# Performance work log

Hardware: AMD Instinct MI355X
Metric: run time of the kernel (lower is better)

## Reference

```python
import jax, jax.numpy as jnp
import numpy as np

N_NODES = 50000


def gat_layer(x, src, dst, W, att_s, att_d, b, concat):
    # PyG GATConv (eval mode): h = x W reshaped to [N, H, C]
    H, C = att_s.shape
    h = (x @ W).reshape(-1, H, C)                      # [N, H, C]
    a_s = (h * att_s).sum(-1)                          # [N, H]
    a_d = (h * att_d).sum(-1)                          # [N, H]
    e = jax.nn.leaky_relu(a_s[src] + a_d[dst], 0.2)    # [E, H]
    # scatter-softmax over destination nodes
    m = jax.ops.segment_max(e, dst, num_segments=N_NODES)
    alpha = jnp.exp(e - m[dst])
    denom = jax.ops.segment_sum(alpha, dst, num_segments=N_NODES)
    alpha = alpha / denom[dst]                         # [E, H]
    msg = h[src] * alpha[:, :, None]                   # [E, H, C]
    out = jax.ops.segment_sum(msg, dst, num_segments=N_NODES)  # [N, H, C]
    out = out.reshape(N_NODES, H * C) if concat else out.mean(axis=1)
    return out + b


def setup_inputs() -> dict:
    key = jax.random.key(0)
    ks = jax.random.split(key, 16)
    F_IN, HID, HEADS, NCLS, E = 512, 64, 4, 40, 800000
    x = jax.random.normal(ks[0], (N_NODES, F_IN), dtype=jnp.float32)
    edge_index = jax.random.randint(ks[1], (2, E), 0, N_NODES, dtype=jnp.int32)

    def glorot(k, shape):
        fan = shape[0]
        return jax.random.normal(k, shape, dtype=jnp.float32) / np.sqrt(fan)

    d1 = HID * HEADS  # 256
    return {
        "x": x,
        "edge_index": edge_index,
        "W1": glorot(ks[2], (F_IN, d1)),
        "as1": glorot(ks[3], (HEADS, HID)),
        "ad1": glorot(ks[4], (HEADS, HID)),
        "b1": jnp.zeros((d1,), jnp.float32),
        "W2": glorot(ks[5], (d1, d1)),
        "as2": glorot(ks[6], (HEADS, HID)),
        "ad2": glorot(ks[7], (HEADS, HID)),
        "b2": jnp.zeros((d1,), jnp.float32),
        "W3": glorot(ks[8], (d1, NCLS)),
        "as3": glorot(ks[9], (1, NCLS)),
        "ad3": glorot(ks[10], (1, NCLS)),
        "b3": jnp.zeros((NCLS,), jnp.float32),
    }


def reference(x, edge_index, W1, as1, ad1, b1, W2, as2, ad2, b2, W3, as3, ad3, b3):
    # add self-loops (PyG GATConv default)
    loops = jnp.arange(N_NODES, dtype=edge_index.dtype)
    src = jnp.concatenate([edge_index[0], loops])
    dst = jnp.concatenate([edge_index[1], loops])
    h = jax.nn.elu(gat_layer(x, src, dst, W1, as1, ad1, b1, True))
    h = jax.nn.elu(gat_layer(h, src, dst, W2, as2, ad2, b2, True))
    out = gat_layer(h, src, dst, W3, as3, ad3, b3, False)
    return out
```

## Files before the change

kernel.cpp:

```cpp
#include <hip/hip_runtime.h>
#include <stdint.h>

#define NN 50000
#define NB 196

typedef unsigned short u16;
typedef _Float16 f16;
typedef __attribute__((ext_vector_type(8))) _Float16 half8;
typedef __attribute__((ext_vector_type(4))) _Float16 half4;
typedef __attribute__((ext_vector_type(4))) float f32x4;

__device__ __forceinline__ void gload_lds16(const void* gsrc, void* ldst){
  __builtin_amdgcn_global_load_lds(
      (const __attribute__((address_space(1))) unsigned int*)gsrc,
      (__attribute__((address_space(3))) unsigned int*)ldst,
      16, 0, 0);
}


__global__ void count_k(const int* __restrict__ dst, int* __restrict__ cnt, int E){
  int i = blockIdx.x * 256 + threadIdx.x;
  int tot = E + NN;
  if (i >= tot) return;
  int d = (i < E) ? dst[i] : (i - E);
  atomicAdd(&cnt[d], 1);
}

__global__ __launch_bounds__(256) void scan_part_k(const int* __restrict__ cnt,
                                                   int* __restrict__ bsum){
  __shared__ int lds[256];
  int tid = threadIdx.x;
  int idx = blockIdx.x * 256 + tid;
  lds[tid] = (idx < NN) ? cnt[idx] : 0;
  __syncthreads();
#pragma unroll
  for (int off = 128; off >= 1; off >>= 1){
    if (tid < off) lds[tid] += lds[tid + off];
    __syncthreads();
  }
  if (tid == 0) bsum[blockIdx.x] = lds[0];
}

__global__ __launch_bounds__(256) void scan_top_k(const int* __restrict__ bsum,
                                                  int* __restrict__ boff,
                                                  int* __restrict__ row_ptr){
  __shared__ int lds[256];
  int tid = threadIdx.x;
  int v = (tid < NB) ? bsum[tid] : 0;
  lds[tid] = v;
  __syncthreads();
#pragma unroll
  for (int off = 1; off < 256; off <<= 1){
    int t = (tid >= off) ? lds[tid - off] : 0;
    __syncthreads();
    lds[tid] += t;
    __syncthreads();
  }
  if (tid < NB) boff[tid] = lds[tid] - v;
  if (tid == 255) row_ptr[NN] = lds[255];
}

__global__ __launch_bounds__(256) void scan_fin_k(const int* __restrict__ cnt,
                                                  const int* __restrict__ boff,
                                                  int* __restrict__ row_ptr,
                                                  int* __restrict__ cursor){
  __shared__ int lds[256];
  int tid = threadIdx.x;
  int idx = blockIdx.x * 256 + tid;
  int v = (idx < NN) ? cnt[idx] : 0;
  lds[tid] = v;
  __syncthreads();
#pragma unroll
  for (int off = 1; off < 256; off <<= 1){
    int t = (tid >= off) ? lds[tid - off] : 0;
    __syncthreads();
    lds[tid] += t;
    __syncthreads();
  }
  if (idx < NN){
    int r = boff[blockIdx.x] + lds[tid] - v;
    row_ptr[idx] = r;
    cursor[idx]  = r;
  }
}

__global__ void scatter_k(const int* __restrict__ src, const int* __restrict__ dst,
                          int* __restrict__ cursor, int* __restrict__ csr, int E){
  int i = blockIdx.x * 256 + threadIdx.x;
  int tot = E + NN;
  if (i >= tot) return;
  int s, d;
  if (i < E){ s = src[i]; d = dst[i]; } else { s = i - E; d = i - E; }
  int pos = atomicAdd(&cursor[d], 1);
  csr[pos] = s;
}


__global__ void transpose_k(const float* __restrict__ W, f16* __restrict__ Wt, int K, int N){
  int i = blockIdx.x * 256 + threadIdx.x;
  if (i >= K * N) return;
  int n = i / K, k = i - n * K;
  Wt[i] = (f16)W[k * N + n];
}


template<bool A_FP32>
__global__ __launch_bounds__(512) void gemm_tile3_k(const void* __restrict__ Aptr,
                                                    const f16* __restrict__ Bt,
                                                    f16* __restrict__ C,
                                                    const float* __restrict__ atts,
                                                    const float* __restrict__ attd,
                                                    float* __restrict__ a_s,
                                                    float* __restrict__ a_d,
                                                    int M, int N, int K){
  constexpr int ABYTES = A_FP32 ? 8192 : 4096;
  constexpr int STEPB  = ABYTES + 8192;
  __shared__ __attribute__((aligned(16))) char lds[2 * STEPB];

  const int tid  = threadIdx.x;
  const int wave = tid >> 6, lane = tid & 63;
  const int quad = lane >> 4, l16 = lane & 15;
  const int wm = wave >> 1, wn = wave & 1;
  const int m0 = blockIdx.x * 64, n0 = blockIdx.y * 128;
  const int sc_l = lane >> 4, r_l = lane & 15;

  size_t bsrc = (size_t)(n0 + wave * 16 + r_l) * K + sc_l * 8;
  const int bdst = wave * 1024;
  size_t asrc; int adst; bool a_active = true;
  {
    int mt = wave & 3;
    int row = m0 + mt * 16 + r_l; if (row > M - 1) row = M - 1;
    if constexpr (A_FP32){
      int hp = wave >> 2;
      asrc = (size_t)row * K + sc_l * 8 + hp * 4;
      adst = hp * 4096 + mt * 1024;
    } else {
      asrc = (size_t)row * K + sc_l * 8;
      adst = mt * 1024;
      a_active = (wave < 4);
    }
  }

  auto stage = [&](int buf, int k0){
    char* Ab = lds + buf * STEPB;
    char* Bb = Ab + ABYTES;
    if constexpr (A_FP32){
      gload_lds16((const float*)Aptr + asrc + k0, Ab + adst);
    } else {
      if (a_active) gload_lds16((const f16*)Aptr + asrc + k0, Ab + adst);
    }
    gload_lds16(Bt + bsrc + k0, Bb + bdst);
  };

  f32x4 acc[4] = {};

  stage(0, 0);
  asm volatile("s_waitcnt vmcnt(0)" ::: "memory");
  __syncthreads();

  const int nk = K >> 5;
  int cur = 0;
  for (int t = 0; t < nk; ++t){
    if (t + 1 < nk) stage(cur ^ 1, (t + 1) << 5);

    char* Ab = lds + cur * STEPB;
    char* Bb = Ab + ABYTES;
    half8 af;
    if constexpr (A_FP32){
      const f32x4 lo = *(const f32x4*)(Ab + (wm * 64 + lane) * 16);
      const f32x4 hi = *(const f32x4*)(Ab + 4096 + (wm * 64 + lane) * 16);
      af[0] = (f16)lo.x; af[1] = (f16)lo.y; af[2] = (f16)lo.z; af[3] = (f16)lo.w;
      af[4] = (f16)hi.x; af[5] = (f16)hi.y; af[6] = (f16)hi.z; af[7] = (f16)hi.w;
    } else {
      af = *(const half8*)(Ab + (wm * 64 + lane) * 16);
    }
    half8 bf[4];
#pragma unroll
    for (int j = 0; j < 4; ++j)
      bf[j] = *(const half8*)(Bb + ((wn * 4 + j) * 64 + lane) * 16);
#pragma unroll
    for (int j = 0; j < 4; ++j)
      acc[j] = __builtin_amdgcn_mfma_f32_16x16x32_f16(af, bf[j], acc[j], 0, 0, 0);

    __syncthreads();
    cur ^= 1;
  }

  const int head = blockIdx.y * 2 + wn;
  float sA[4], dA[4];
#pragma unroll
  for (int j = 0; j < 4; ++j){
    sA[j] = atts[head * 64 + j * 16 + l16];
    dA[j] = attd[head * 64 + j * 16 + l16];
  }
#pragma unroll
  for (int r = 0; r < 4; ++r){
    int mm = m0 + wm * 16 + quad * 4 + r;
    float vs = 0.f, vd = 0.f;
#pragma unroll
    for (int j = 0; j < 4; ++j){
      float v = acc[j][r];
      vs += v * sA[j];
      vd += v * dA[j];
      int n = n0 + (wn * 4 + j) * 16 + l16;
      if (mm < M) C[(size_t)mm * N + n] = (f16)v;
    }
#pragma unroll
    for (int off = 8; off >= 1; off >>= 1){
      vs += __shfl_xor(vs, off);
      vd += __shfl_xor(vd, off);
    }
    if (l16 == 0 && mm < M){
      a_s[mm * 4 + head] = vs;
      a_d[mm * 4 + head] = vd;
    }
  }
}


__global__ __launch_bounds__(256) void gemm_n40_k(const f16* __restrict__ A,
                                                  const f16* __restrict__ Bt,
                                                  f16* __restrict__ C,
                                                  const float* __restrict__ atts,
                                                  const float* __restrict__ attd,
                                                  float* __restrict__ a_s,
                                                  float* __restrict__ a_d,
                                                  int M, int K){
  constexpr int ABYTES = 4096;
  constexpr int BBYTES = 3072;
  constexpr int STEPB  = ABYTES + BBYTES;
  __shared__ __attribute__((aligned(16))) char lds[2 * STEPB];

  const int tid  = threadIdx.x;
  const int wave = tid >> 6, lane = tid & 63;
  const int quad = lane >> 4, l16 = lane & 15;
  const int m0 = blockIdx.x * 64;
  const int sc_l = lane >> 4, r_l = lane & 15;

  int arow = m0 + wave * 16 + r_l; if (arow > M - 1) arow = M - 1;
  const size_t asrc = (size_t)arow * K + sc_l * 8;
  const int adst = wave * 1024;
  int brow = wave * 16 + r_l; if (brow > 39) brow = 39;
  const size_t bsrc = (size_t)brow * K + sc_l * 8;
  const int bdst = wave * 1024;
  const bool b_active = (wave < 3);

  auto stage = [&](int buf, int k0){
    char* Ab = lds + buf * STEPB;
    char* Bb = Ab + ABYTES;
    gload_lds16(A + asrc + k0, Ab + adst);
    if (b_active) gload_lds16(Bt + bsrc + k0, Bb + bdst);
  };

  f32x4 acc[3] = {};
  stage(0, 0);
  asm volatile("s_waitcnt vmcnt(0)" ::: "memory");
  __syncthreads();

  const int nk = K >> 5;
  int cur = 0;
  for (int t = 0; t < nk; ++t){
    if (t + 1 < nk) stage(cur ^ 1, (t + 1) << 5);
    char* Ab = lds + cur * STEPB;
    char* Bb = Ab + ABYTES;
    half8 af = *(const half8*)(Ab + (wave * 64 + lane) * 16);
    half8 bf[3];
#pragma unroll
    for (int j = 0; j < 3; ++j)
      bf[j] = *(const half8*)(Bb + (j * 64 + lane) * 16);
#pragma unroll
    for (int j = 0; j < 3; ++j)
      acc[j] = __builtin_amdgcn_mfma_f32_16x16x32_f16(af, bf[j], acc[j], 0, 0, 0);
    __syncthreads();
    cur ^= 1;
  }

  float sA[3], dA[3];
#pragma unroll
  for (int j = 0; j < 3; ++j){
    int n = j * 16 + l16;
    sA[j] = (n < 40) ? atts[n] : 0.f;
    dA[j] = (n < 40) ? attd[n] : 0.f;
  }
#pragma unroll
  for (int r = 0; r < 4; ++r){
    int mm = m0 + wave * 16 + quad * 4 + r;
    float vs = 0.f, vd = 0.f;
#pragma unroll
    for (int j = 0; j < 3; ++j){
      float v = acc[j][r];
      vs += v * sA[j];
      vd += v * dA[j];
      int n = j * 16 + l16;
      if (mm < M && n < 40) C[(size_t)mm * 40 + n] = (f16)v;
    }
#pragma unroll
    for (int off = 8; off >= 1; off >>= 1){
      vs += __shfl_xor(vs, off);
      vd += __shfl_xor(vd, off);
    }
    if (l16 == 0 && mm < M){
      a_s[mm] = vs;
      a_d[mm] = vd;
    }
  }
}


__device__ __forceinline__ float lrelu(float e){ return e > 0.f ? e : 0.2f * e; }

__global__ __launch_bounds__(256) void agg4_k(const f16* __restrict__ h,
                                              const float* __restrict__ a_s,
                                              const float* __restrict__ a_d,
                                              const int* __restrict__ row_ptr,
                                              const int* __restrict__ csr,
                                              const float* __restrict__ bias,
                                              f16* __restrict__ out){
  int w = blockIdx.x * 4 + (threadIdx.x >> 6);
  if (w >= NN) return;
  const int lane = threadIdx.x & 63;
  const int head = lane >> 4;
  const char* hb = (const char*)h;
  const uint32_t hoff_lane = (uint32_t)lane << 3;
  const float ad = a_d[w * 4 + head];
  const int beg = row_ptr[w], end = row_ptr[w + 1], endm1 = end - 1;

  float denom = 0.f, acc0 = 0.f, acc1 = 0.f, acc2 = 0.f, acc3 = 0.f;

  float ce[4]; half4 chv[4];
  float ne[4]; half4 nhv[4];

  auto ldgrp = [&](int base, float* EV, half4* HV){
#pragma unroll
    for (int q = 0; q < 4; ++q){
      int idx = base + q; idx = idx < endm1 ? idx : endm1;
      int s = csr[idx];
      EV[q] = a_s[(s << 2) + head];
      HV[q] = *(const half4*)(hb + (((uint32_t)s << 9) | hoff_lane));
    }
  };

  ldgrp(beg, ce, chv);
  int base = beg;
  while (true){
    bool more = base + 4 < end;
    if (more) ldgrp(base + 4, ne, nhv);
    int rem = end - base;
#pragma unroll
    for (int q = 0; q < 4; ++q){
      float al = __expf(lrelu(ce[q] + ad));
      al = (q < rem) ? al : 0.f;
      denom += al;
      acc0 += al * (float)chv[q].x;
      acc1 += al * (float)chv[q].y;
      acc2 += al * (float)chv[q].z;
      acc3 += al * (float)chv[q].w;
    }
    if (!more) break;
#pragma unroll
    for (int q = 0; q < 4; ++q){ ce[q] = ne[q]; chv[q] = nhv[q]; }
    base += 4;
  }

  float inv = 1.f / fmaxf(denom, 1e-30f);
  float o0 = acc0 * inv + bias[lane * 4 + 0];
  float o1 = acc1 * inv + bias[lane * 4 + 1];
  float o2 = acc2 * inv + bias[lane * 4 + 2];
  float o3 = acc3 * inv + bias[lane * 4 + 3];
  o0 = o0 > 0.f ? o0 : __expf(o0) - 1.f;
  o1 = o1 > 0.f ? o1 : __expf(o1) - 1.f;
  o2 = o2 > 0.f ? o2 : __expf(o2) - 1.f;
  o3 = o3 > 0.f ? o3 : __expf(o3) - 1.f;
  half4 r; r.x = (f16)o0; r.y = (f16)o1; r.z = (f16)o2; r.w = (f16)o3;
  *(half4*)(out + (size_t)w * 256 + lane * 4) = r;
}

__global__ __launch_bounds__(256) void agg1_k(const f16* __restrict__ h,
                                              const float* __restrict__ a_s,
                                              const float* __restrict__ a_d,
                                              const int* __restrict__ row_ptr,
                                              const int* __restrict__ csr,
                                              const float* __restrict__ bias,
                                              float* __restrict__ out){
  int w = blockIdx.x * 4 + (threadIdx.x >> 6);
  if (w >= NN) return;
  const int lane = threadIdx.x & 63;
  const int cl = (lane < 40) ? lane : 0;
  const float ad = a_d[w];
  const int beg = row_ptr[w], end = row_ptr[w + 1], endm1 = end - 1;

  float denom = 0.f, acc = 0.f;
  float ce[4], chv[4];
  float ne[4], nhv[4];

  auto ldgrp = [&](int base, float* EV, float* HV){
#pragma unroll
    for (int q = 0; q < 4; ++q){
      int idx = base + q; idx = idx < endm1 ? idx : endm1;
      int s = csr[idx];
      EV[q] = a_s[s];
      HV[q] = (float)h[(size_t)s * 40 + cl];
    }
  };

  ldgrp(beg, ce, chv);
  int base = beg;
  while (true){
    bool more = base + 4 < end;
    if (more) ldgrp(base + 4, ne, nhv);
    int rem = end - base;
#pragma unroll
    for (int q = 0; q < 4; ++q){
      float al = __expf(lrelu(ce[q] + ad));
      al = (q < rem) ? al : 0.f;
      denom += al;
      acc += al * chv[q];
    }
    if (!more) break;
#pragma unroll
    for (int q = 0; q < 4; ++q){ ce[q] = ne[q]; chv[q] = nhv[q]; }
    base += 4;
  }

  if (lane < 40){
    float o = acc / fmaxf(denom, 1e-30f) + bias[lane];
    out[(size_t)w * 40 + lane] = o;
  }
}


extern "C" void kernel_launch(void* const* d_in, const int* in_sizes, int n_in,
                              void* d_out, int out_size, void* d_ws, size_t ws_size,
                              hipStream_t stream){
  const float* x   = (const float*)d_in[0];
  const int*   ei  = (const int*)d_in[1];
  const float* W1  = (const float*)d_in[2];
  const float* as1 = (const float*)d_in[3];
  const float* ad1 = (const float*)d_in[4];
  const float* b1  = (const float*)d_in[5];
  const float* W2  = (const float*)d_in[6];
  const float* as2 = (const float*)d_in[7];
  const float* ad2 = (const float*)d_in[8];
  const float* b2  = (const float*)d_in[9];
  const float* W3  = (const float*)d_in[10];
  const float* as3 = (const float*)d_in[11];
  const float* ad3 = (const float*)d_in[12];
  const float* b3  = (const float*)d_in[13];

  const int E = in_sizes[1] / 2;
  const int ETOT = E + NN;
  const int* src_arr = ei;
  const int* dst_arr = ei + E;

  char* ws = (char*)d_ws;
  size_t off = 0;
  auto alloc = [&](size_t bytes) -> void* {
    void* p = ws + off; off += (bytes + 255) & ~(size_t)255; return p;
  };
  int*   cnt     = (int*)  alloc((size_t)NN * 4);
  int*   row_ptr = (int*)  alloc((size_t)(NN + 1) * 4);
  int*   cursor  = (int*)  alloc((size_t)NN * 4);
  int*   csr     = (int*)  alloc((size_t)ETOT * 4);
  int*   bsum    = (int*)  alloc((size_t)256 * 4);
  int*   boff    = (int*)  alloc((size_t)256 * 4);
  f16*   W1t     = (f16*)  alloc((size_t)512 * 256 * 2);
  f16*   W2t     = (f16*)  alloc((size_t)256 * 256 * 2);
  f16*   W3t     = (f16*)  alloc((size_t)256 * 40 * 2);
  float* a_s     = (float*)alloc((size_t)NN * 4 * 4);
  float* a_d     = (float*)alloc((size_t)NN * 4 * 4);
  f16*   hbuf    = (f16*)  alloc((size_t)NN * 256 * 2);
  f16*   xbuf    = (f16*)  alloc((size_t)NN * 256 * 2);
  (void)ws_size; (void)n_in; (void)out_size;

  hipMemsetAsync(cnt, 0, (size_t)NN * 4, stream);
  int egrid = (ETOT + 255) / 256;
  count_k    <<<egrid, 256, 0, stream>>>(dst_arr, cnt, E);
  scan_part_k<<<NB, 256, 0, stream>>>(cnt, bsum);
  scan_top_k <<<1, 256, 0, stream>>>(bsum, boff, row_ptr);
  scan_fin_k <<<NB, 256, 0, stream>>>(cnt, boff, row_ptr, cursor);
  scatter_k  <<<egrid, 256, 0, stream>>>(src_arr, dst_arr, cursor, csr, E);

  transpose_k<<<(512 * 256 + 255) / 256, 256, 0, stream>>>(W1, W1t, 512, 256);
  transpose_k<<<(256 * 256 + 255) / 256, 256, 0, stream>>>(W2, W2t, 256, 256);
  transpose_k<<<(256 * 40  + 255) / 256, 256, 0, stream>>>(W3, W3t, 256, 40);

  dim3 blk512(512);
  dim3 blk(256);
  dim3 gT((NN + 63) / 64, 2);
  dim3 gC((NN + 63) / 64, 1);
  int nodeblocks = (NN + 3) / 4;

  gemm_tile3_k<true> <<<gT, blk512, 0, stream>>>(x, W1t, hbuf, as1, ad1, a_s, a_d, NN, 256, 512);
  agg4_k <<<nodeblocks, blk, 0, stream>>>(hbuf, a_s, a_d, row_ptr, csr, b1, xbuf);

  gemm_tile3_k<false><<<gT, blk512, 0, stream>>>(xbuf, W2t, hbuf, as2, ad2, a_s, a_d, NN, 256, 256);
  agg4_k <<<nodeblocks, blk, 0, stream>>>(hbuf, a_s, a_d, row_ptr, csr, b2, xbuf);

  gemm_n40_k<<<gC, blk, 0, stream>>>(xbuf, W3t, hbuf, as3, ad3, a_s, a_d, NN, 256);
  agg1_k <<<nodeblocks, blk, 0, stream>>>(hbuf, a_s, a_d, row_ptr, csr, b3, (float*)d_out);
}
```

Before: 534.1 us.

## Replace LDS-staged GEMMs with direct register-prefetched global loads

The three GEMM kernels no longer stage A and B tiles through LDS with async global-to-LDS loads and block barriers. Each lane now loads its MFMA fragments straight from global memory into registers, with one-step register prefetch and a fully unrolled compile-time K loop. The big GEMMs also move from 512-thread 64x128 tiles to 256-thread 32x128 tiles. This removes LDS traffic and __syncthreads, but each wave now fetches its own B fragments, so reuse moves from LDS to the cache hierarchy and global load volume may rise.

Measured after the change: 643.4 us. 1.2x slower.

```diff
diff --git a/kernel.cpp b/kernel.cpp
--- a/kernel.cpp
+++ b/kernel.cpp
@@ -9,13 +9,6 @@
 typedef __attribute__((ext_vector_type(8))) _Float16 half8;
 typedef __attribute__((ext_vector_type(4))) _Float16 half4;
 typedef __attribute__((ext_vector_type(4))) float f32x4;
-
-__device__ __forceinline__ void gload_lds16(const void* gsrc, void* ldst){
-  __builtin_amdgcn_global_load_lds(
-      (const __attribute__((address_space(1))) unsigned int*)gsrc,
-      (__attribute__((address_space(3))) unsigned int*)ldst,
-      16, 0, 0);
-}
 
 
 __global__ void count_k(const int* __restrict__ dst, int* __restrict__ cnt, int E){
@@ -104,89 +97,78 @@
 }
 
 
-template<bool A_FP32>
-__global__ __launch_bounds__(512) void gemm_tile3_k(const void* __restrict__ Aptr,
-                                                    const f16* __restrict__ Bt,
-                                                    f16* __restrict__ C,
-                                                    const float* __restrict__ atts,
-                                                    const float* __restrict__ attd,
-                                                    float* __restrict__ a_s,
-                                                    float* __restrict__ a_d,
-                                                    int M, int N, int K){
-  constexpr int ABYTES = A_FP32 ? 8192 : 4096;
-  constexpr int STEPB  = ABYTES + 8192;
-  __shared__ __attribute__((aligned(16))) char lds[2 * STEPB];
-
+template<bool A_FP32, int K>
+__global__ __launch_bounds__(256) void gemm_direct_k(const void* __restrict__ Aptr,
+                                                     const f16* __restrict__ Bt,
+                                                     f16* __restrict__ C,
+                                                     const float* __restrict__ atts,
+                                                     const float* __restrict__ attd,
+                                                     float* __restrict__ a_s,
+                                                     float* __restrict__ a_d,
+                                                     int M){
+  constexpr int NK = K / 32;
+  constexpr int N  = 256;
   const int tid  = threadIdx.x;
   const int wave = tid >> 6, lane = tid & 63;
   const int quad = lane >> 4, l16 = lane & 15;
   const int wm = wave >> 1, wn = wave & 1;
-  const int m0 = blockIdx.x * 64, n0 = blockIdx.y * 128;
-  const int sc_l = lane >> 4, r_l = lane & 15;
-
-  size_t bsrc = (size_t)(n0 + wave * 16 + r_l) * K + sc_l * 8;
-  const int bdst = wave * 1024;
-  size_t asrc; int adst; bool a_active = true;
-  {
-    int mt = wave & 3;
-    int row = m0 + mt * 16 + r_l; if (row > M - 1) row = M - 1;
-    if constexpr (A_FP32){
-      int hp = wave >> 2;
-      asrc = (size_t)row * K + sc_l * 8 + hp * 4;
-      adst = hp * 4096 + mt * 1024;
-    } else {
-      asrc = (size_t)row * K + sc_l * 8;
-      adst = mt * 1024;
-      a_active = (wave < 4);
-    }
-  }
-
-  auto stage = [&](int buf, int k0){
-    char* Ab = lds + buf * STEPB;
-    char* Bb = Ab + ABYTES;
-    if constexpr (A_FP32){
-      gload_lds16((const float*)Aptr + asrc + k0, Ab + adst);
-    } else {
-      if (a_active) gload_lds16((const f16*)Aptr + asrc + k0, Ab + adst);
-    }
-    gload_lds16(Bt + bsrc + k0, Bb + bdst);
-  };
+  const int bid = blockIdx.x;
+  const int m0 = (bid >> 1) * 32;
+  const int n0 = (bid & 1) * 128;
+  const int r  = lane & 15, ck = lane >> 4;
+
+  int arow = m0 + wm * 16 + r; if (arow > M - 1) arow = M - 1;
+  const float* A32 = (const float*)Aptr;
+  const f16*   A16 = (const f16*)Aptr;
+  const size_t abase = (size_t)arow * K + ck * 8;
+  size_t bbase[4];
+#pragma unroll
+  for (int j = 0; j < 4; ++j)
+    bbase[j] = (size_t)(n0 + wn * 64 + j * 16 + r) * K + ck * 8;
 
   f32x4 acc[4] = {};
 
-  stage(0, 0);
-  asm volatile("s_waitcnt vmcnt(0)" ::: "memory");
-  __syncthreads();
-
-  const int nk = K >> 5;
-  int cur = 0;
-  for (int t = 0; t < nk; ++t){
-    if (t + 1 < nk) stage(cur ^ 1, (t + 1) << 5);
-
-    char* Ab = lds + cur * STEPB;
-    char* Bb = Ab + ABYTES;
+  f32x4 plo = {}, phi = {}; half8 pa = {};
+  half8 pb[4];
+  if constexpr (A_FP32){
+    plo = *(const f32x4*)(A32 + abase);
+    phi = *(const f32x4*)(A32 + abase + 4);
+  } else {
+    pa = *(const half8*)(A16 + abase);
+  }
+#pragma unroll
+  for (int j = 0; j < 4; ++j) pb[j] = *(const half8*)(Bt + bbase[j]);
+
+#pragma unroll
+  for (int t = 0; t < NK; ++t){
+    f32x4 nlo = {}, nhi = {}; half8 na = {}; half8 nb[4] = {};
+    if (t + 1 < NK){
+      const int ko = (t + 1) * 32;
+      if constexpr (A_FP32){
+        nlo = *(const f32x4*)(A32 + abase + ko);
+        nhi = *(const f32x4*)(A32 + abase + ko + 4);
+      } else {
+        na = *(const half8*)(A16 + abase + ko);
+      }
+#pragma unroll
+      for (int j = 0; j < 4; ++j) nb[j] = *(const half8*)(Bt + bbase[j] + ko);
+    }
     half8 af;
     if constexpr (A_FP32){
-      const f32x4 lo = *(const f32x4*)(Ab + (wm * 64 + lane) * 16);
-      const f32x4 hi = *(const f32x4*)(Ab + 4096 + (wm * 64 + lane) * 16);
-      af[0] = (f16)lo.x; af[1] = (f16)lo.y; af[2] = (f16)lo.z; af[3] = (f16)lo.w;
-      af[4] = (f16)hi.x; af[5] = (f16)hi.y; af[6] = (f16)hi.z; af[7] = (f16)hi.w;
+      af[0] = (f16)plo.x; af[1] = (f16)plo.y; af[2] = (f16)plo.z; af[3] = (f16)plo.w;
+      af[4] = (f16)phi.x; af[5] = (f16)phi.y; af[6] = (f16)phi.z; af[7] = (f16)phi.w;
     } else {
-      af = *(const half8*)(Ab + (wm * 64 + lane) * 16);
-    }
-    half8 bf[4];
+      af = pa;
+    }
 #pragma unroll
     for (int j = 0; j < 4; ++j)
-      bf[j] = *(const half8*)(Bb + ((wn * 4 + j) * 64 + lane) * 16);
-#pragma unroll
-    for (int j = 0; j < 4; ++j)
-      acc[j] = __builtin_amdgcn_mfma_f32_16x16x32_f16(af, bf[j], acc[j], 0, 0, 0);
-
-    __syncthreads();
-    cur ^= 1;
-  }
-
-  const int head = blockIdx.y * 2 + wn;
+      acc[j] = __builtin_amdgcn_mfma_f32_16x16x32_f16(af, pb[j], acc[j], 0, 0, 0);
+    plo = nlo; phi = nhi; pa = na;
+#pragma unroll
+    for (int j = 0; j < 4; ++j) pb[j] = nb[j];
+  }
+
+  const int head = (bid & 1) * 2 + wn;
   float sA[4], dA[4];
 #pragma unroll
   for (int j = 0; j < 4; ++j){
@@ -194,12 +176,12 @@
     dA[j] = attd[head * 64 + j * 16 + l16];
   }
 #pragma unroll
-  for (int r = 0; r < 4; ++r){
-    int mm = m0 + wm * 16 + quad * 4 + r;
+  for (int rr = 0; rr < 4; ++rr){
+    int mm = m0 + wm * 16 + quad * 4 + rr;
     float vs = 0.f, vd = 0.f;
 #pragma unroll
     for (int j = 0; j < 4; ++j){
-      float v = acc[j][r];
+      float v = acc[j][rr];
       vs += v * sA[j];
       vd += v * dA[j];
       int n = n0 + (wn * 4 + j) * 16 + l16;
@@ -218,61 +200,52 @@
 }
 
 
-__global__ __launch_bounds__(256) void gemm_n40_k(const f16* __restrict__ A,
-                                                  const f16* __restrict__ Bt,
-                                                  f16* __restrict__ C,
-                                                  const float* __restrict__ atts,
-                                                  const float* __restrict__ attd,
-                                                  float* __restrict__ a_s,
-                                                  float* __restrict__ a_d,
-                                                  int M, int K){
-  constexpr int ABYTES = 4096;
-  constexpr int BBYTES = 3072;
-  constexpr int STEPB  = ABYTES + BBYTES;
-  __shared__ __attribute__((aligned(16))) char lds[2 * STEPB];
-
+__global__ __launch_bounds__(256) void gemm_n40d_k(const f16* __restrict__ A,
+                                                   const f16* __restrict__ Bt,
+                                                   f16* __restrict__ C,
+                                                   const float* __restrict__ atts,
+                                                   const float* __restrict__ attd,
+                                                   float* __restrict__ a_s,
+                                                   float* __restrict__ a_d,
+                                                   int M){
+  constexpr int K = 256, NK = K / 32;
   const int tid  = threadIdx.x;
   const int wave = tid >> 6, lane = tid & 63;
   const int quad = lane >> 4, l16 = lane & 15;
   const int m0 = blockIdx.x * 64;
-  const int sc_l = lane >> 4, r_l = lane & 15;
-
-  int arow = m0 + wave * 16 + r_l; if (arow > M - 1) arow = M - 1;
-  const size_t asrc = (size_t)arow * K + sc_l * 8;
-  const int adst = wave * 1024;
-  int brow = wave * 16 + r_l; if (brow > 39) brow = 39;
-  const size_t bsrc = (size_t)brow * K + sc_l * 8;
-  const int bdst = wave * 1024;
-  const bool b_active = (wave < 3);
-
-  auto stage = [&](int buf, int k0){
-    char* Ab = lds + buf * STEPB;
-    char* Bb = Ab + ABYTES;
-    gload_lds16(A + asrc + k0, Ab + adst);
-    if (b_active) gload_lds16(Bt + bsrc + k0, Bb + bdst);
-  };
+  const int r  = lane & 15, ck = lane >> 4;
+
+  int arow = m0 + wave * 16 + r; if (arow > M - 1) arow = M - 1;
+  const size_t abase = (size_t)arow * K + ck * 8;
+  size_t bbase[3];
+#pragma unroll
+  for (int j = 0; j < 3; ++j){
+    int brow = j * 16 + r; if (brow > 39) brow = 39;
+    bbase[j] = (size_t)brow * K + ck * 8;
+  }
 
   f32x4 acc[3] = {};
-  stage(0, 0);
-  asm volatile("s_waitcnt vmcnt(0)" ::: "memory");
-  __syncthreads();
-
-  const int nk = K >> 5;
-  int cur = 0;
-  for (int t = 0; t < nk; ++t){
-    if (t + 1 < nk) stage(cur ^ 1, (t + 1) << 5);
-    char* Ab = lds + cur * STEPB;
-    char* Bb = Ab + ABYTES;
-    half8 af = *(const half8*)(Ab + (wave * 64 + lane) * 16);
-    half8 bf[3];
+
+  half8 pa = *(const half8*)(A + abase);
+  half8 pb[3];
+#pragma unroll
+  for (int j = 0; j < 3; ++j) pb[j] = *(const half8*)(Bt + bbase[j]);
+
+#pragma unroll
+  for (int t = 0; t < NK; ++t){
+    half8 na = {}; half8 nb[3] = {};
+    if (t + 1 < NK){
+      const int ko = (t + 1) * 32;
+      na = *(const half8*)(A + abase + ko);
+#pragma unroll
+      for (int j = 0; j < 3; ++j) nb[j] = *(const half8*)(Bt + bbase[j] + ko);
+    }
 #pragma unroll
     for (int j = 0; j < 3; ++j)
-      bf[j] = *(const half8*)(Bb + (j * 64 + lane) * 16);
-#pragma unroll
-    for (int j = 0; j < 3; ++j)
-      acc[j] = __builtin_amdgcn_mfma_f32_16x16x32_f16(af, bf[j], acc[j], 0, 0, 0);
-    __syncthreads();
-    cur ^= 1;
+      acc[j] = __builtin_amdgcn_mfma_f32_16x16x32_f16(pa, pb[j], acc[j], 0, 0, 0);
+    pa = na;
+#pragma unroll
+    for (int j = 0; j < 3; ++j) pb[j] = nb[j];
   }
 
   float sA[3], dA[3];
@@ -283,12 +256,12 @@
     dA[j] = (n < 40) ? attd[n] : 0.f;
   }
 #pragma unroll
-  for (int r = 0; r < 4; ++r){
-    int mm = m0 + wave * 16 + quad * 4 + r;
+  for (int rr = 0; rr < 4; ++rr){
+    int mm = m0 + wave * 16 + quad * 4 + rr;
     float vs = 0.f, vd = 0.f;
 #pragma unroll
     for (int j = 0; j < 3; ++j){
-      float v = acc[j][r];
+      float v = acc[j][rr];
       vs += v * sA[j];
       vd += v * dA[j];
       int n = j * 16 + l16;
@@ -371,8 +344,8 @@
   o1 = o1 > 0.f ? o1 : __expf(o1) - 1.f;
   o2 = o2 > 0.f ? o2 : __expf(o2) - 1.f;
   o3 = o3 > 0.f ? o3 : __expf(o3) - 1.f;
-  half4 r; r.x = (f16)o0; r.y = (f16)o1; r.z = (f16)o2; r.w = (f16)o3;
-  *(half4*)(out + (size_t)w * 256 + lane * 4) = r;
+  half4 rv; rv.x = (f16)o0; rv.y = (f16)o1; rv.z = (f16)o2; rv.w = (f16)o3;
+  *(half4*)(out + (size_t)w * 256 + lane * 4) = rv;
 }
 
 __global__ __launch_bounds__(256) void agg1_k(const f16* __restrict__ h,
@@ -484,18 +457,17 @@
   transpose_k<<<(256 * 256 + 255) / 256, 256, 0, stream>>>(W2, W2t, 256, 256);
   transpose_k<<<(256 * 40  + 255) / 256, 256, 0, stream>>>(W3, W3t, 256, 40);
 
-  dim3 blk512(512);
   dim3 blk(256);
-  dim3 gT((NN + 63) / 64, 2);
+  const int gD = ((NN + 31) / 32) * 2;
   dim3 gC((NN + 63) / 64, 1);
   int nodeblocks = (NN + 3) / 4;
 
-  gemm_tile3_k<true> <<<gT, blk512, 0, stream>>>(x, W1t, hbuf, as1, ad1, a_s, a_d, NN, 256, 512);
-  agg4_k <<<nodeblocks, blk, 0, stream>>>(hbuf, a_s, a_d, row_ptr, csr, b1, xbuf);
-
-  gemm_tile3_k<false><<<gT, blk512, 0, stream>>>(xbuf, W2t, hbuf, as2, ad2, a_s, a_d, NN, 256, 256);
-  agg4_k <<<nodeblocks, blk, 0, stream>>>(hbuf, a_s, a_d, row_ptr, csr, b2, xbuf);
-
-  gemm_n40_k<<<gC, blk, 0, stream>>>(xbuf, W3t, hbuf, as3, ad3, a_s, a_d, NN, 256);
-  agg1_k <<<nodeblocks, blk, 0, stream>>>(hbuf, a_s, a_d, row_ptr, csr, b3, (float*)d_out);
-}
+  gemm_direct_k<true, 512><<<gD, blk, 0, stream>>>(x, W1t, hbuf, as1, ad1, a_s, a_d, NN);
+  agg4_k<<<nodeblocks, blk, 0, stream>>>(hbuf, a_s, a_d, row_ptr, csr, b1, xbuf);
+
+  gemm_direct_k<false, 256><<<gD, blk, 0, stream>>>(xbuf, W2t, hbuf, as2, ad2, a_s, a_d, NN);
+  agg4_k<<<nodeblocks, blk, 0, stream>>>(hbuf, a_s, a_d, row_ptr, csr, b2, xbuf);
+
+  gemm_n40d_k<<<gC, blk, 0, stream>>>(xbuf, W3t, hbuf, as3, ad3, a_s, a_d, NN);
+  agg1_k<<<nodeblocks, blk, 0, stream>>>(hbuf, a_s, a_d, row_ptr, csr, b3, (float*)d_out);
+}
```

## Replace double-buffered GEMM staging with four-slot LDS ring and vmcnt-based waits

Applied to the files above, without the earlier changes.

The two GEMM kernels move from a double buffer with a full vmcnt(0) drain each step to a four-slot LDS ring that keeps three global-to-LDS loads in flight. Explicit s_waitcnt vmcnt(N) counters replace the drain, with s_barrier before each compute and lgkmcnt(0) plus a barrier after it. This is meant to hide global-load latency behind MFMA work, at the cost of doubling LDS per block, which could lower occupancy. The GEMMs are only part of a pipeline dominated by the aggregation kernels.

Measured after the change: 534.3 us. About the same (+0.0%).

```diff
diff --git a/kernel.cpp b/kernel.cpp
--- a/kernel.cpp
+++ b/kernel.cpp
@@ -16,6 +16,10 @@
       (__attribute__((address_space(3))) unsigned int*)ldst,
       16, 0, 0);
 }
+
+#define VMW(N)  asm volatile("s_waitcnt vmcnt(" #N ")" ::: "memory")
+#define LGKM0() asm volatile("s_waitcnt lgkmcnt(0)" ::: "memory")
+#define BARR()  asm volatile("s_barrier" ::: "memory")
 
 
 __global__ void count_k(const int* __restrict__ dst, int* __restrict__ cnt, int E){
@@ -105,17 +109,17 @@
 
 
 template<bool A_FP32>
-__global__ __launch_bounds__(512) void gemm_tile3_k(const void* __restrict__ Aptr,
-                                                    const f16* __restrict__ Bt,
-                                                    f16* __restrict__ C,
-                                                    const float* __restrict__ atts,
-                                                    const float* __restrict__ attd,
-                                                    float* __restrict__ a_s,
-                                                    float* __restrict__ a_d,
-                                                    int M, int N, int K){
+__global__ __launch_bounds__(512) void gemm_ring_k(const void* __restrict__ Aptr,
+                                                   const f16* __restrict__ Bt,
+                                                   f16* __restrict__ C,
+                                                   const float* __restrict__ atts,
+                                                   const float* __restrict__ attd,
+                                                   float* __restrict__ a_s,
+                                                   float* __restrict__ a_d,
+                                                   int M, int K){
   constexpr int ABYTES = A_FP32 ? 8192 : 4096;
   constexpr int STEPB  = ABYTES + 8192;
-  __shared__ __attribute__((aligned(16))) char lds[2 * STEPB];
+  __shared__ __attribute__((aligned(16))) char lds[4 * STEPB];
 
   const int tid  = threadIdx.x;
   const int wave = tid >> 6, lane = tid & 63;
@@ -140,6 +144,7 @@
       a_active = (wave < 4);
     }
   }
+  const bool two_ops = A_FP32 ? true : (wave < 4);
 
   auto stage = [&](int buf, int k0){
     char* Ab = lds + buf * STEPB;
@@ -154,16 +159,8 @@
 
   f32x4 acc[4] = {};
 
-  stage(0, 0);
-  asm volatile("s_waitcnt vmcnt(0)" ::: "memory");
-  __syncthreads();
-
-  const int nk = K >> 5;
-  int cur = 0;
-  for (int t = 0; t < nk; ++t){
-    if (t + 1 < nk) stage(cur ^ 1, (t + 1) << 5);
-
-    char* Ab = lds + cur * STEPB;
+  auto compute = [&](int buf){
+    char* Ab = lds + buf * STEPB;
     char* Bb = Ab + ABYTES;
     half8 af;
     if constexpr (A_FP32){
@@ -181,11 +178,27 @@
 #pragma unroll
     for (int j = 0; j < 4; ++j)
       acc[j] = __builtin_amdgcn_mfma_f32_16x16x32_f16(af, bf[j], acc[j], 0, 0, 0);
-
-    __syncthreads();
-    cur ^= 1;
-  }
-
+  };
+
+  stage(0, 0); stage(1, 32); stage(2, 64);
+
+  const int nk = K >> 5;
+  for (int t = 0; t < nk - 3; ++t){
+    stage((t + 3) & 3, (t + 3) << 5);
+    if (two_ops) VMW(6); else VMW(3);
+    BARR();
+    compute(t & 3);
+    LGKM0();
+    BARR();
+  }
+  if (two_ops) VMW(4); else VMW(2);
+  BARR(); compute((nk - 3) & 3);
+  if (two_ops) VMW(2); else VMW(1);
+  BARR(); compute((nk - 2) & 3);
+  VMW(0);
+  BARR(); compute((nk - 1) & 3);
+
+  const int N = 256;
   const int head = blockIdx.y * 2 + wn;
   float sA[4], dA[4];
 #pragma unroll
@@ -229,7 +242,7 @@
   constexpr int ABYTES = 4096;
   constexpr int BBYTES = 3072;
   constexpr int STEPB  = ABYTES + BBYTES;
-  __shared__ __attribute__((aligned(16))) char lds[2 * STEPB];
+  __shared__ __attribute__((aligned(16))) char lds[4 * STEPB];
 
   const int tid  = threadIdx.x;
   const int wave = tid >> 6, lane = tid & 63;
@@ -244,6 +257,7 @@
   const size_t bsrc = (size_t)brow * K + sc_l * 8;
   const int bdst = wave * 1024;
   const bool b_active = (wave < 3);
+  const bool two_ops = b_active;
 
   auto stage = [&](int buf, int k0){
     char* Ab = lds + buf * STEPB;
@@ -253,15 +267,8 @@
   };
 
   f32x4 acc[3] = {};
-  stage(0, 0);
-  asm volatile("s_waitcnt vmcnt(0)" ::: "memory");
-  __syncthreads();
-
-  const int nk = K >> 5;
-  int cur = 0;
-  for (int t = 0; t < nk; ++t){
-    if (t + 1 < nk) stage(cur ^ 1, (t + 1) << 5);
-    char* Ab = lds + cur * STEPB;
+  auto compute = [&](int buf){
+    char* Ab = lds + buf * STEPB;
     char* Bb = Ab + ABYTES;
     half8 af = *(const half8*)(Ab + (wave * 64 + lane) * 16);
     half8 bf[3];
@@ -271,9 +278,24 @@
 #pragma unroll
     for (int j = 0; j < 3; ++j)
       acc[j] = __builtin_amdgcn_mfma_f32_16x16x32_f16(af, bf[j], acc[j], 0, 0, 0);
-    __syncthreads();
-    cur ^= 1;
-  }
+  };
+
+  stage(0, 0); stage(1, 32); stage(2, 64);
+  const int nk = K >> 5;
+  for (int t = 0; t < nk - 3; ++t){
+    stage((t + 3) & 3, (t + 3) << 5);
+    if (two_ops) VMW(6); else VMW(3);
+    BARR();
+    compute(t & 3);
+    LGKM0();
+    BARR();
+  }
+  if (two_ops) VMW(4); else VMW(2);
+  BARR(); compute((nk - 3) & 3);
+  if (two_ops) VMW(2); else VMW(1);
+  BARR(); compute((nk - 2) & 3);
+  VMW(0);
+  BARR(); compute((nk - 1) & 3);
 
   float sA[3], dA[3];
 #pragma unroll
@@ -371,8 +393,8 @@
   o1 = o1 > 0.f ? o1 : __expf(o1) - 1.f;
   o2 = o2 > 0.f ? o2 : __expf(o2) - 1.f;
   o3 = o3 > 0.f ? o3 : __expf(o3) - 1.f;
-  half4 r; r.x = (f16)o0; r.y = (f16)o1; r.z = (f16)o2; r.w = (f16)o3;
-  *(half4*)(out + (size_t)w * 256 + lane * 4) = r;
+  half4 rv; rv.x = (f16)o0; rv.y = (f16)o1; rv.z = (f16)o2; rv.w = (f16)o3;
+  *(half4*)(out + (size_t)w * 256 + lane * 4) = rv;
 }
 
 __global__ __launch_bounds__(256) void agg1_k(const f16* __restrict__ h,
@@ -490,12 +512,12 @@
   dim3 gC((NN + 63) / 64, 1);
   int nodeblocks = (NN + 3) / 4;
 
-  gemm_tile3_k<true> <<<gT, blk512, 0, stream>>>(x, W1t, hbuf, as1, ad1, a_s, a_d, NN, 256, 512);
-  agg4_k <<<nodeblocks, blk, 0, stream>>>(hbuf, a_s, a_d, row_ptr, csr, b1, xbuf);
-
-  gemm_tile3_k<false><<<gT, blk512, 0, stream>>>(xbuf, W2t, hbuf, as2, ad2, a_s, a_d, NN, 256, 256);
-  agg4_k <<<nodeblocks, blk, 0, stream>>>(hbuf, a_s, a_d, row_ptr, csr, b2, xbuf);
+  gemm_ring_k<true> <<<gT, blk512, 0, stream>>>(x, W1t, hbuf, as1, ad1, a_s, a_d, NN, 512);
+  agg4_k<<<nodeblocks, blk, 0, stream>>>(hbuf, a_s, a_d, row_ptr, csr, b1, xbuf);
+
+  gemm_ring_k<false><<<gT, blk512, 0, stream>>>(xbuf, W2t, hbuf, as2, ad2, a_s, a_d, NN, 256);
+  agg4_k<<<nodeblocks, blk, 0, stream>>>(hbuf, a_s, a_d, row_ptr, csr, b2, xbuf);
 
   gemm_n40_k<<<gC, blk, 0, stream>>>(xbuf, W3t, hbuf, as3, ad3, a_s, a_d, NN, 256);
-  agg1_k <<<nodeblocks, blk, 0, stream>>>(hbuf, a_s, a_d, row_ptr, csr, b3, (float*)d_out);
-}
+  agg1_k<<<nodeblocks, blk, 0, stream>>>(hbuf, a_s, a_d, row_ptr, csr, b3, (float*)d_out);
+}
```
